# Optimization experiments

Measured on AMD Instinct MI355X. Metric: run time of the kernel, lower is better.

The kernel has to match this reference:

```python
import jax, jax.numpy as jnp
import numpy as np

MAX_TOTAL = 20        # max_total_size
MAX_PER_CLASS = 20    # max_output_size_per_class
SCORE_TH = 0.5        # score_threshold
IOU_TH = 0.5          # tf combined NMS default iou_threshold
K_CAND = 200          # top candidates per class considered for NMS
VARIANCES = jnp.array([0.1, 0.1, 0.2, 0.2], jnp.float32)


def setup_inputs() -> dict:
    key = jax.random.key(0)
    k1, k2, k3, k4, k5, k6 = jax.random.split(key, 6)
    B, N, C = 64, 8732, 21
    pred_deltas = jax.random.normal(k1, (B, N, 4), jnp.float32)
    pred_labels = jax.random.uniform(k2, (B, N, C), dtype=jnp.float32)
    # synthetic normalized anchors (y1,x1,y2,x2) with valid extents
    cy = jax.random.uniform(k3, (N,), dtype=jnp.float32)
    cx = jax.random.uniform(k4, (N,), dtype=jnp.float32)
    h = jax.random.uniform(k5, (N,), dtype=jnp.float32, minval=0.05, maxval=0.3)
    w = jax.random.uniform(k6, (N,), dtype=jnp.float32, minval=0.05, maxval=0.3)
    anchors = jnp.stack([cy - h / 2, cx - w / 2, cy + h / 2, cx + w / 2], axis=-1)
    return {"pred_deltas": pred_deltas, "pred_labels": pred_labels, "anchors": anchors}


def _decode(anchors, deltas):
    # anchors [N,4] (y1,x1,y2,x2); deltas [B,N,4] (dy,dx,dh,dw) -> boxes [B,N,4]
    ah = anchors[:, 2] - anchors[:, 0]
    aw = anchors[:, 3] - anchors[:, 1]
    acy = anchors[:, 0] + 0.5 * ah
    acx = anchors[:, 1] + 0.5 * aw
    cy = deltas[..., 0] * ah + acy
    cx = deltas[..., 1] * aw + acx
    h = jnp.exp(deltas[..., 2]) * ah
    w = jnp.exp(deltas[..., 3]) * aw
    return jnp.stack([cy - 0.5 * h, cx - 0.5 * w, cy + 0.5 * h, cx + 0.5 * w], axis=-1)


def _pairwise_iou(boxes):
    # boxes [K,4] -> iou [K,K]
    y1, x1, y2, x2 = boxes[:, 0], boxes[:, 1], boxes[:, 2], boxes[:, 3]
    area = (y2 - y1) * (x2 - x1)
    ih = jnp.clip(jnp.minimum(y2[:, None], y2[None, :]) - jnp.maximum(y1[:, None], y1[None, :]), 0.0)
    iw = jnp.clip(jnp.minimum(x2[:, None], x2[None, :]) - jnp.maximum(x1[:, None], x1[None, :]), 0.0)
    inter = ih * iw
    return inter / (area[:, None] + area[None, :] - inter + 1e-8)


def _nms_one_class(scores, boxes):
    # scores [N], boxes [N,4] -> (top scores [MAX_PER_CLASS], boxes [MAX_PER_CLASS,4])
    vals, idx = jax.lax.top_k(scores, K_CAND)          # sorted desc
    cboxes = boxes[idx]                                # [K,4]
    iou = _pairwise_iou(cboxes)                        # [K,K]
    valid = vals > SCORE_TH
    ar = jnp.arange(K_CAND)

    def body(i, keep):
        suppressed = jnp.any(keep & (iou[i] > IOU_TH) & (ar < i))
        return keep.at[i].set(valid[i] & ~suppressed)

    keep = jax.lax.fori_loop(0, K_CAND, body, jnp.zeros(K_CAND, dtype=bool))
    kept_scores = jnp.where(keep, vals, 0.0)
    top_vals, top_i = jax.lax.top_k(kept_scores, MAX_PER_CLASS)
    return top_vals, cboxes[top_i]


def reference(pred_deltas, pred_labels, anchors):
    deltas = pred_deltas * VARIANCES                       # variance scaling
    boxes = _decode(anchors, deltas)                       # [B,N,4]
    # zero out all class scores where argmax class == 0 (background)
    lab_map = jnp.argmax(pred_labels, axis=-1, keepdims=True)
    scores = jnp.where(lab_map != 0, pred_labels, 0.0)     # [B,N,C]

    per_class = jax.vmap(_nms_one_class, in_axes=(1, None))   # over classes
    per_batch = jax.vmap(per_class, in_axes=(0, 0))           # over batch
    cls_scores, cls_boxes = per_batch(scores, boxes)          # [B,C,P], [B,C,P,4]

    B, C, P = cls_scores.shape
    flat_scores = cls_scores.reshape(B, C * P)
    flat_boxes = cls_boxes.reshape(B, C * P, 4)
    class_ids = jnp.broadcast_to(jnp.arange(C, dtype=jnp.float32)[:, None], (C, P)).reshape(-1)

    top_vals, top_i = jax.lax.top_k(flat_scores, MAX_TOTAL)   # [B,MAX_TOTAL]
    final_boxes = jnp.take_along_axis(flat_boxes, top_i[..., None], axis=1)
    final_boxes = jnp.clip(final_boxes, 0.0, 1.0)             # combined NMS clip_boxes=True
    valid = top_vals > 0.0
    final_boxes = jnp.where(valid[..., None], final_boxes, 0.0)
    final_labels = jnp.where(valid, class_ids[top_i], 0.0)
    return final_boxes, top_vals, final_labels
```

## Files before the change

kernel.cpp:

```cpp
#include <hip/hip_runtime.h>
#include <stdint.h>

typedef unsigned long long u64;
typedef unsigned int u32;
typedef unsigned short u16;

#define BATCH 64
#define NANCH 8732
#define NCHUNK 1092
#define NCLS 21
#define KCAND 200
#define CAP 2048
#define PPC 20
#define PTOT 20
#define PRETHR 0.9f
#define HWIN 1792

__global__ __launch_bounds__(256) void kdecode(
    const float* __restrict__ labels,
    unsigned char* __restrict__ msk, u64* __restrict__ lists,
    u32* __restrict__ cnt, int useT)
{
#pragma clang fp contract(off)
    const int n = blockIdx.x * 256 + threadIdx.x;
    const int b = blockIdx.y;
    const int lane = threadIdx.x & 63;
    const bool active = (n < NANCH);

    float v[NCLS];
#pragma unroll
    for (int c = 0; c < NCLS; ++c) v[c] = 0.0f;
    bool mk = false;
    if (active) {
        const float* lab = labels + ((size_t)b * NANCH + n) * NCLS;
#pragma unroll
        for (int c = 0; c < NCLS; ++c) v[c] = lab[c];
        float mx = v[0]; int am = 0;
#pragma unroll
        for (int c = 1; c < NCLS; ++c) if (v[c] > mx) { mx = v[c]; am = c; }
        mk = (am != 0);
        msk[(size_t)b * NANCH + n] = mk ? 1 : 0;
    }
    if (!useT) return;

    u32 myHits = 0;
#pragma unroll
    for (int c = 0; c < NCLS; ++c)
        if (active && mk && v[c] >= PRETHR) myHits |= (1u << c);

    u32 myCnt = 0;
#pragma unroll
    for (int c = 0; c < NCLS; ++c) {
        u64 m = __ballot((myHits >> c) & 1u);
        if (lane == c) myCnt = (u32)__popcll(m);
    }
    u32 myBase = 0;
    if (lane < NCLS) myBase = atomicAdd(&cnt[b * NCLS + lane], myCnt);

#pragma unroll
    for (int c = 0; c < NCLS; ++c) {
        u64 m = __ballot((myHits >> c) & 1u);
        u32 base = (u32)__shfl((int)myBase, c, 64);
        if ((m >> lane) & 1ull) {
            u32 rank = (u32)__popcll(m & ((1ull << lane) - 1ull));
            u32 slot = base + rank;
            if (slot < CAP)
                lists[((size_t)b * NCLS + c) * CAP + slot] =
                    ((u64)__float_as_uint(v[c]) << 32) | (u32)(~(u32)n);
        }
    }
}

__device__ __forceinline__ u64 shflxor64(u64 x, int m) {
    return (u64)__shfl_xor((long long)x, m, 64);
}

__device__ __forceinline__ void suffixFind(const u32* hist, u32* waveTot, int nb, int need,
                                           int* sSel, int* sAbove, int* sH, int* sTot,
                                           int tid, int lane, int wv)
{
    int K = (nb + 255) >> 8;
    int base = tid * K;
    u32 own = 0;
    for (int q = 0; q < K; ++q) { int bi = base + q; own += (bi < nb) ? hist[bi] : 0u; }
    u32 s = own;
#pragma unroll
    for (int d = 1; d < 64; d <<= 1) {
        u32 o = __shfl_down(s, d, 64);
        if (lane + d < 64) s += o;
    }
    if (lane == 0) waveTot[wv] = s;
    __syncthreads();
    if (tid == 0 && sTot) *sTot = (int)(waveTot[0] + waveTot[1] + waveTot[2] + waveTot[3]);
    u32 add = 0;
    for (int w = wv + 1; w < 4; ++w) add += waveTot[w];
    u32 cum = (s - own) + add;
    for (int q = K - 1; q >= 0; --q) {
        int bi = base + q;
        u32 hh = (bi < nb) ? hist[bi] : 0u;
        if (cum < (u32)need && cum + hh >= (u32)need) { *sSel = bi; *sAbove = (int)cum; *sH = (int)hh; }
        cum += hh;
    }
    __syncthreads();
}

__global__ __launch_bounds__(256) void knms(
    const float* __restrict__ labels, const unsigned char* __restrict__ msk,
    const u64* __restrict__ lists, const u32* __restrict__ cnt,
    const float* __restrict__ deltas, const float* __restrict__ anchors,
    float* __restrict__ clsScores, float* __restrict__ clsBoxes, int useT)
{
#pragma clang fp contract(off)
    __shared__ __align__(16) char smem[8192];
    u32*   hist = (u32*)smem;
    float* cbY1 = (float*)smem;
    float* cbX1 = (float*)(smem + 1024);
    float* cbY2 = (float*)(smem + 2048);
    float* cbX2 = (float*)(smem + 3072);
    float* cbAr = (float*)(smem + 4096);
    float* cVal = (float*)(smem + 5120);
    u64*   iouT = (u64*)(smem + 6144);
    __shared__ u64 candKey[256];
    __shared__ u32 waveTot[4];
    __shared__ float outS[PPC];
    __shared__ float outB[PPC * 4];
    __shared__ int sSel, sAbove, sH, sTot, sN, sKP;

    const int tid = threadIdx.x;
    const int lane = tid & 63;
    const int wv = tid >> 6;
    const int bc = blockIdx.x;
    const int b = bc / NCLS;
    const int c = bc % NCLS;

    const int nTHR = useT ? (int)cnt[bc] : -1;
    const bool fast = useT && (nTHR >= KCAND) && (nTHR <= CAP);

    if (fast) {
        const u64* lst = lists + (size_t)bc * CAP;
        u64 kr[8];
#pragma unroll
        for (int q = 0; q < 8; ++q) {
            int i = q * 256 + tid;
            kr[q] = (i < nTHR) ? lst[i] : 0ull;
        }
        hist[tid] = 0;
        if (tid == 0) { sSel = -1; sAbove = 0; sH = 0; sN = 0; sKP = 0; }
        __syncthreads();
#pragma unroll
        for (int q = 0; q < 8; ++q) {
            if (q * 256 + tid < nTHR) {
                float v = __uint_as_float((u32)(kr[q] >> 32));
                u32 t = (u32)(v * 65536.0f);
                atomicAdd(&hist[(t >> 5) - HWIN], 1u);
            }
        }
        __syncthreads();
        suffixFind(hist, waveTot, 256, KCAND, &sSel, &sAbove, &sH, nullptr, tid, lane, wv);
        int A = sAbove;
        u32 T16 = (u32)(HWIN + sSel) << 5;
        int cnt2 = A + sH;

        if (cnt2 > 256) {
            if (tid < 32) hist[tid] = 0;
            if (tid == 0) { sSel = -1; sAbove = 0; sH = 0; }
            __syncthreads();
#pragma unroll
            for (int q = 0; q < 8; ++q) {
                if (q * 256 + tid < nTHR) {
                    float v = __uint_as_float((u32)(kr[q] >> 32));
                    u32 t = (u32)(v * 65536.0f);
                    if (t >= T16 && t < T16 + 32) atomicAdd(&hist[t - T16], 1u);
                }
            }
            __syncthreads();
            suffixFind(hist, waveTot, 32, KCAND - A, &sSel, &sAbove, &sH, nullptr, tid, lane, wv);
            A += sAbove;
            T16 += (u32)sSel;
        }
#pragma unroll
        for (int q = 0; q < 8; ++q) {
            int i = q * 256 + tid;
            bool pred = (i < nTHR);
            if (pred) {
                float v = __uint_as_float((u32)(kr[q] >> 32));
                pred = ((u32)(v * 65536.0f) >= T16);
            }
            u64 m = __ballot(pred);
            if (m) {
                int base = 0;
                if (lane == 0) base = atomicAdd(&sN, (int)__popcll(m));
                base = __shfl(base, 0, 64);
                if (pred) {
                    int slot = base + (int)__popcll(m & ((1ull << lane) - 1ull));
                    if (slot < 256) candKey[slot] = kr[q];
                }
            }
        }
    } else {
        uint4 rc[5];
        for (int q = 0; q < 5; ++q) {
            int chunk = q * 256 + tid;
            u32 w4[4] = {0, 0, 0, 0};
            if (chunk < NCHUNK) {
                for (int w = 0; w < 4; ++w)
                    for (int h = 0; h < 2; ++h) {
                        int n = chunk * 8 + w * 2 + h;
                        u32 t = 0;
                        if (n < NANCH && msk[(size_t)b * NANCH + n]) {
                            float v = labels[((size_t)b * NANCH + n) * NCLS + c];
                            t = (u32)(v * 65536.0f);
                        }
                        w4[w] |= t << (16 * h);
                    }
            }
            rc[q] = make_uint4(w4[0], w4[1], w4[2], w4[3]);
        }
        for (int q = tid; q < 1024; q += 256) hist[1024 + q] = 0;
        if (tid == 0) { sSel = -1; sAbove = 0; sH = 0; sTot = 0; sN = 0; sKP = 0; }
        __syncthreads();
#pragma unroll
        for (int q = 0; q < 5; ++q) {
            if (q * 256 + tid < NCHUNK) {
                u32 w4[4] = {rc[q].x, rc[q].y, rc[q].z, rc[q].w};
#pragma unroll
                for (int w = 0; w < 4; ++w) {
                    u32 lo = w4[w] & 0xFFFFu, hi = w4[w] >> 16;
                    if (lo & 0x8000u) atomicAdd(&hist[lo >> 5], 1u);
                    if (hi & 0x8000u) atomicAdd(&hist[hi >> 5], 1u);
                }
            }
        }
        __syncthreads();
        suffixFind(hist + 1024, waveTot, 1024, KCAND, &sSel, &sAbove, &sH, &sTot, tid, lane, wv);
        int A; int cnt2; u32 T16;
        if (sTot < KCAND) { T16 = 32768u; A = 0; cnt2 = sTot; }
        else { A = sAbove; T16 = (u32)(1024 + sSel) << 5; cnt2 = A + sH; }
        if (cnt2 > 256) {
            if (tid < 32) hist[tid] = 0;
            if (tid == 0) { sSel = -1; sAbove = 0; sH = 0; }
            __syncthreads();
#pragma unroll
            for (int q = 0; q < 5; ++q) {
                if (q * 256 + tid < NCHUNK) {
                    u32 w4[4] = {rc[q].x, rc[q].y, rc[q].z, rc[q].w};
#pragma unroll
                    for (int w = 0; w < 4; ++w) {
                        u32 lo = w4[w] & 0xFFFFu, hi = w4[w] >> 16;
                        if (lo >= T16 && lo < T16 + 32) atomicAdd(&hist[lo - T16], 1u);
                        if (hi >= T16 && hi < T16 + 32) atomicAdd(&hist[hi - T16], 1u);
                    }
                }
            }
            __syncthreads();
            suffixFind(hist, waveTot, 32, KCAND - A, &sSel, &sAbove, &sH, nullptr, tid, lane, wv);
            A += sAbove;
            T16 += (u32)sSel;
        }
#pragma unroll
        for (int q = 0; q < 5; ++q) {
            int chunk = q * 256 + tid;
            if (chunk < NCHUNK) {
                u32 w4[4] = {rc[q].x, rc[q].y, rc[q].z, rc[q].w};
#pragma unroll
                for (int w = 0; w < 4; ++w) {
#pragma unroll
                    for (int h = 0; h < 2; ++h) {
                        u32 t = (h == 0) ? (w4[w] & 0xFFFFu) : (w4[w] >> 16);
                        if (t >= T16) {
                            int n = chunk * 8 + w * 2 + h;
                            float v = labels[((size_t)b * NANCH + n) * NCLS + c];
                            int slot = atomicAdd(&sN, 1);
                            if (slot < 256)
                                candKey[slot] = ((u64)__float_as_uint(v) << 32) | (u32)(~(u32)n);
                        }
                    }
                }
            }
        }
    }
    __syncthreads();
    int nc = sN; if (nc > 256) nc = 256;

    u64 x = (tid < nc) ? candKey[tid] : 0ull;
    for (int k = 2; k <= 256; k <<= 1) {
        for (int j = k >> 1; j > 0; j >>= 1) {
            u64 y;
            if (j < 64) {
                y = shflxor64(x, j);
            } else {
                __syncthreads();
                candKey[tid] = x;
                __syncthreads();
                y = candKey[tid ^ j];
            }
            bool keepMax = ((tid & k) == 0) == ((tid & j) == 0);
            u64 mx = (x > y) ? x : y;
            u64 mn = (x > y) ? y : x;
            x = keepMax ? mx : mn;
        }
    }

    float myV = __uint_as_float((u32)(x >> 32));
    float myY1 = 0.f, myX1 = 0.f, myY2 = 0.f, myX2 = 0.f, myAr = 0.f;
    u32 idx = ~(u32)x;
    if (tid < KCAND && idx < (u32)NANCH) {
        float4 d = ((const float4*)deltas)[(size_t)b * NANCH + idx];
        float4 a = ((const float4*)anchors)[idx];
        float ah = a.z - a.x, aw = a.w - a.y;
        float acy = a.x + 0.5f * ah, acx = a.y + 0.5f * aw;
        float cy = (d.x * 0.1f) * ah + acy;
        float cx = (d.y * 0.1f) * aw + acx;
        float hh2 = expf(d.z * 0.2f) * ah;
        float ww2 = expf(d.w * 0.2f) * aw;
        myY1 = cy - 0.5f * hh2; myX1 = cx - 0.5f * ww2;
        myY2 = cy + 0.5f * hh2; myX2 = cx + 0.5f * ww2;
        myAr = (myY2 - myY1) * (myX2 - myX1);
    } else {
        myV = 0.f;
    }
    __syncthreads();
    cbY1[tid] = myY1; cbX1[tid] = myX1; cbY2[tid] = myY2; cbX2[tid] = myX2;
    cbAr[tid] = myAr; cVal[tid] = myV;

    u64 k0 = 0, k1 = 0, k2 = 0, k3 = 0;
    int KPw = 0;
    for (int t0 = 0; t0 < 4; ++t0) {
        __syncthreads();
        if (sKP >= PPC) break;
        int rowBase = t0 * 64;
        int rows = KCAND - rowBase; if (rows > 64) rows = 64;
        for (int r = wv; r < rows; r += 4) {
            int i = rowBase + r;
            float y1i = cbY1[i], x1i = cbX1[i], y2i = cbY2[i], x2i = cbX2[i], ari = cbAr[i];
            for (int cg = 0; cg <= t0; ++cg) {
                int j = cg * 64 + lane;
                float ih = fminf(y2i, cbY2[j]) - fmaxf(y1i, cbY1[j]);
                ih = fmaxf(ih, 0.0f);
                float iw = fminf(x2i, cbX2[j]) - fmaxf(x1i, cbX1[j]);
                iw = fmaxf(iw, 0.0f);
                float inter = ih * iw;
                float iou = inter / (ari + cbAr[j] - inter + 1e-8f);
                u64 bal = __ballot(iou > 0.5f);
                if (lane == 0) iouT[r * 4 + cg] = bal;
            }
        }
        __syncthreads();
        if (tid < 64) {
            int i = rowBase + lane;
            u64 r0 = 0, r1 = 0, r2 = 0, r3 = 0;
            bool vld = false;
            if (lane < rows) {
                r0 = iouT[lane * 4 + 0]; r1 = iouT[lane * 4 + 1];
                r2 = iouT[lane * 4 + 2]; r3 = iouT[lane * 4 + 3];
                vld = cVal[i] > 0.5f;
            }
            for (int l = 0; l < rows; ++l) {
                int mydec = (vld && !((k0 & r0) | (k1 & r1) | (k2 & r2) | (k3 & r3))) ? 1 : 0;
                int d = __shfl(mydec, l, 64);
                if (d) {
                    u64 bit = 1ull << l;
                    if (t0 == 0) k0 |= bit; else if (t0 == 1) k1 |= bit;
                    else if (t0 == 2) k2 |= bit; else k3 |= bit;
                    ++KPw;
                    if (KPw >= PPC) break;
                }
            }
            if (tid == 0) sKP = KPw;
        }
    }
    __syncthreads();

    if (tid < PPC) outS[tid] = 0.0f;
    if (tid < PPC * 4) outB[tid] = 0.0f;
    __syncthreads();

    if (tid < 64) {
        int base = 0;
#pragma unroll
        for (int chunk = 0; chunk < 4; ++chunk) {
            u64 kw = (chunk == 0) ? k0 : (chunk == 1) ? k1 : (chunk == 2) ? k2 : k3;
            int i = chunk * 64 + tid;
            bool kept = ((kw >> tid) & 1ull) != 0;
            int rank = base + (int)__popcll(kw & ((1ull << tid) - 1ull));
            if (kept && rank < PPC && i < KCAND) {
                outS[rank] = cVal[i];
                outB[rank * 4 + 0] = cbY1[i];
                outB[rank * 4 + 1] = cbX1[i];
                outB[rank * 4 + 2] = cbY2[i];
                outB[rank * 4 + 3] = cbX2[i];
            }
            base += (int)__popcll(kw);
        }
    }
    __syncthreads();
    if (tid < PPC) clsScores[(size_t)bc * PPC + tid] = outS[tid];
    if (tid < PPC * 4) clsBoxes[(size_t)bc * PPC * 4 + tid] = outB[tid];
}

__global__ __launch_bounds__(512) void kmerge(
    const float* __restrict__ clsScores, const float* __restrict__ clsBoxes,
    float* __restrict__ out)
{
#pragma clang fp contract(off)
    __shared__ u64 key[512];
    const int tid = threadIdx.x;
    const int b = blockIdx.x;
    const int F = NCLS * PPC;
    u64 x = 0;
    if (tid < F) {
        float v = clsScores[(size_t)b * F + tid];
        x = ((u64)__float_as_uint(v) << 32) | (u32)(~(u32)tid);
    }
    for (int k = 2; k <= 512; k <<= 1) {
        for (int j = k >> 1; j >= 1; j >>= 1) {
            u64 y;
            if (j < 64) {
                y = shflxor64(x, j);
            } else {
                __syncthreads();
                key[tid] = x;
                __syncthreads();
                y = key[tid ^ j];
            }
            bool keepMax = ((tid & k) == 0) == ((tid & j) == 0);
            u64 mx = x > y ? x : y;
            u64 mn = x > y ? y : x;
            x = keepMax ? mx : mn;
        }
    }
    if (tid < PTOT) {
        float v = __uint_as_float((u32)(x >> 32));
        u32 f = ~((u32)x);
        bool valid = (v > 0.0f) && (f < (u32)F);
        float cls = valid ? (float)(f / PPC) : 0.0f;
        float* oB = out;
        float* oV = out + (size_t)BATCH * PTOT * 4;
        float* oL = oV + (size_t)BATCH * PTOT;
#pragma unroll
        for (int q = 0; q < 4; ++q) {
            float xq = 0.0f;
            if (valid) {
                xq = clsBoxes[((size_t)b * F + f) * 4 + q];
                xq = fminf(fmaxf(xq, 0.0f), 1.0f);
            }
            oB[((size_t)b * PTOT + tid) * 4 + q] = xq;
        }
        oV[(size_t)b * PTOT + tid] = v;
        oL[(size_t)b * PTOT + tid] = cls;
    }
}

extern "C" void kernel_launch(void* const* d_in, const int* in_sizes, int n_in,
                              void* d_out, int out_size, void* d_ws, size_t ws_size,
                              hipStream_t stream)
{
    const float* deltas  = (const float*)d_in[0];
    const float* labels  = (const float*)d_in[1];
    const float* anchors = (const float*)d_in[2];
    float* out = (float*)d_out;
    char* ws = (char*)d_ws;

    const size_t mskOff  = 0;
    const size_t cntOff  = 558848;
    const size_t csOff   = 564480;
    const size_t cbOff   = 672000;
    const size_t listOff = 1102336;
    const size_t needT   = 23122432;

    unsigned char* msk = (unsigned char*)(ws + mskOff);
    u32* cnt         = (u32*)(ws + cntOff);
    float* clsScores = (float*)(ws + csOff);
    float* clsBoxes  = (float*)(ws + cbOff);
    u64* lists       = (u64*)(ws + listOff);
    int useT = (ws_size >= needT) ? 1 : 0;

    if (useT) hipMemsetAsync(cnt, 0, BATCH * NCLS * sizeof(u32), stream);
    dim3 gA((NANCH + 255) / 256, BATCH);
    kdecode<<<gA, 256, 0, stream>>>(labels, msk, lists, cnt, useT);
    knms<<<BATCH * NCLS, 256, 0, stream>>>(labels, msk, lists, cnt, deltas, anchors,
                                           clsScores, clsBoxes, useT);
    kmerge<<<BATCH, 512, 0, stream>>>(clsScores, clsBoxes, out);
}
```

Before: 58.43 us.

## Replace histogram select and bitonic sort with rank-by-counting on fast path

Raises the prefilter threshold so each batch-class list holds fewer candidates, then caps the fast path at 512 entries. Within that path, the two-pass histogram threshold search and the bitonic sort are replaced by a counting rank. Each thread compares its two keys against all 512 in shared memory and scatters them straight into sorted position. This removes the atomics, the suffix scans and the many barriers of the sort. In exchange it adds O(512) shared-memory reads per thread, and any list above 512 entries falls back to the slow full-scan path.

```diff
diff --git a/kernel.cpp b/kernel.cpp
--- a/kernel.cpp
+++ b/kernel.cpp
@@ -11,10 +11,10 @@
 #define NCLS 21
 #define KCAND 200
 #define CAP 2048
+#define RANKN 512
 #define PPC 20
 #define PTOT 20
-#define PRETHR 0.9f
-#define HWIN 1792
+#define PRETHR 0.96f
 
 __global__ __launch_bounds__(256) void kdecode(
     const float* __restrict__ labels,
@@ -112,6 +112,7 @@
 {
 #pragma clang fp contract(off)
     __shared__ __align__(16) char smem[8192];
+    u64*   keys = (u64*)smem;
     u32*   hist = (u32*)smem;
     float* cbY1 = (float*)smem;
     float* cbX1 = (float*)(smem + 1024);
@@ -134,69 +135,32 @@
     const int c = bc % NCLS;
 
     const int nTHR = useT ? (int)cnt[bc] : -1;
-    const bool fast = useT && (nTHR >= KCAND) && (nTHR <= CAP);
-
+    const bool fast = useT && (nTHR >= KCAND) && (nTHR <= RANKN);
+
+    u64 x;
     if (fast) {
         const u64* lst = lists + (size_t)bc * CAP;
-        u64 kr[8];
-#pragma unroll
-        for (int q = 0; q < 8; ++q) {
-            int i = q * 256 + tid;
-            kr[q] = (i < nTHR) ? lst[i] : 0ull;
-        }
-        hist[tid] = 0;
-        if (tid == 0) { sSel = -1; sAbove = 0; sH = 0; sN = 0; sKP = 0; }
-        __syncthreads();
-#pragma unroll
-        for (int q = 0; q < 8; ++q) {
-            if (q * 256 + tid < nTHR) {
-                float v = __uint_as_float((u32)(kr[q] >> 32));
-                u32 t = (u32)(v * 65536.0f);
-                atomicAdd(&hist[(t >> 5) - HWIN], 1u);
-            }
-        }
-        __syncthreads();
-        suffixFind(hist, waveTot, 256, KCAND, &sSel, &sAbove, &sH, nullptr, tid, lane, wv);
-        int A = sAbove;
-        u32 T16 = (u32)(HWIN + sSel) << 5;
-        int cnt2 = A + sH;
-
-        if (cnt2 > 256) {
-            if (tid < 32) hist[tid] = 0;
-            if (tid == 0) { sSel = -1; sAbove = 0; sH = 0; }
-            __syncthreads();
-#pragma unroll
-            for (int q = 0; q < 8; ++q) {
-                if (q * 256 + tid < nTHR) {
-                    float v = __uint_as_float((u32)(kr[q] >> 32));
-                    u32 t = (u32)(v * 65536.0f);
-                    if (t >= T16 && t < T16 + 32) atomicAdd(&hist[t - T16], 1u);
-                }
-            }
-            __syncthreads();
-            suffixFind(hist, waveTot, 32, KCAND - A, &sSel, &sAbove, &sH, nullptr, tid, lane, wv);
-            A += sAbove;
-            T16 += (u32)sSel;
-        }
-#pragma unroll
-        for (int q = 0; q < 8; ++q) {
-            int i = q * 256 + tid;
-            bool pred = (i < nTHR);
-            if (pred) {
-                float v = __uint_as_float((u32)(kr[q] >> 32));
-                pred = ((u32)(v * 65536.0f) >= T16);
-            }
-            u64 m = __ballot(pred);
-            if (m) {
-                int base = 0;
-                if (lane == 0) base = atomicAdd(&sN, (int)__popcll(m));
-                base = __shfl(base, 0, 64);
-                if (pred) {
-                    int slot = base + (int)__popcll(m & ((1ull << lane) - 1ull));
-                    if (slot < 256) candKey[slot] = kr[q];
-                }
-            }
-        }
+        keys[tid] = (tid < nTHR) ? lst[tid] : 0ull;
+        {
+            int i = 256 + tid;
+            keys[i] = (i < nTHR) ? lst[i] : 0ull;
+        }
+        candKey[tid] = 0ull;
+        if (tid == 0) sKP = 0;
+        __syncthreads();
+        u64 myK0 = keys[tid], myK1 = keys[256 + tid];
+        int r0 = 0, r1 = 0;
+#pragma unroll 8
+        for (int i = 0; i < RANKN; ++i) {
+            u64 kk = keys[i];
+            r0 += (kk > myK0) ? 1 : 0;
+            r1 += (kk > myK1) ? 1 : 0;
+        }
+        __syncthreads();
+        if (tid < nTHR && r0 < 256) candKey[r0] = myK0;
+        if (256 + tid < nTHR && r1 < 256) candKey[r1] = myK1;
+        __syncthreads();
+        x = candKey[tid];
     } else {
         uint4 rc[5];
         for (int q = 0; q < 5; ++q) {
@@ -278,26 +242,25 @@
                 }
             }
         }
-    }
-    __syncthreads();
-    int nc = sN; if (nc > 256) nc = 256;
-
-    u64 x = (tid < nc) ? candKey[tid] : 0ull;
-    for (int k = 2; k <= 256; k <<= 1) {
-        for (int j = k >> 1; j > 0; j >>= 1) {
-            u64 y;
-            if (j < 64) {
-                y = shflxor64(x, j);
-            } else {
-                __syncthreads();
-                candKey[tid] = x;
-                __syncthreads();
-                y = candKey[tid ^ j];
-            }
-            bool keepMax = ((tid & k) == 0) == ((tid & j) == 0);
-            u64 mx = (x > y) ? x : y;
-            u64 mn = (x > y) ? y : x;
-            x = keepMax ? mx : mn;
+        __syncthreads();
+        int nc = sN; if (nc > 256) nc = 256;
+        x = (tid < nc) ? candKey[tid] : 0ull;
+        for (int k = 2; k <= 256; k <<= 1) {
+            for (int j = k >> 1; j > 0; j >>= 1) {
+                u64 y;
+                if (j < 64) {
+                    y = shflxor64(x, j);
+                } else {
+                    __syncthreads();
+                    candKey[tid] = x;
+                    __syncthreads();
+                    y = candKey[tid ^ j];
+                }
+                bool keepMax = ((tid & k) == 0) == ((tid & j) == 0);
+                u64 mx = (x > y) ? x : y;
+                u64 mn = (x > y) ? y : x;
+                x = keepMax ? mx : mn;
+            }
         }
     }
 
```

After: 92.45 us. 58.2% more time.
